# Kernel optimization log

Measured on AMD Instinct MI355X. Metric: run time of the kernel, lower is better.

The kernel has to match this reference:

```python
import jax, jax.numpy as jnp
import numpy as np

# Config from the repo: 128^3 volume, patch 2 -> 64^3 patches, embed_dim 64
D = H = W = 64
C = 64
WS = 2        # window_size
SS = 1        # shift_size
NH = 8        # num_heads
MLP = 256     # num_mlp
B = 2
L = D * H * W
S = WS ** 3   # tokens per window = 8
NUM_REL = (2 * WS - 1) ** 3  # 27


def _rel_position_index(ws):
    # faithful to source, incl. np.meshgrid default 'xy' indexing
    coords = np.stack(np.meshgrid(np.arange(ws), np.arange(ws), np.arange(ws)))
    cf = coords.reshape(3, -1)
    rc = (cf[:, :, None] - cf[:, None, :]).transpose(1, 2, 0)
    rc[:, :, 0] += ws - 1
    rc[:, :, 1] += ws - 1
    rc[:, :, 2] += ws - 1
    rc[:, :, 0] *= 2 * ws - 1
    return rc.sum(-1)  # (S, S) int


def _attn_mask(d, h, w, ws, ss):
    sl = (slice(0, -ws), slice(-ws, -ss), slice(-ss, None))
    m = np.zeros((1, d, h, w, 1), np.float32)
    cnt = 0
    for ds in sl:
        for hs in sl:
            for wsl in sl:
                m[:, ds, hs, wsl, :] = cnt
                cnt += 1
    pz, py, px = d // ws, h // ws, w // ws
    mw = m.reshape(1, pz, ws, py, ws, px, ws, 1)
    mw = mw.transpose(0, 1, 3, 5, 2, 4, 6, 7).reshape(-1, ws ** 3)  # (nW, S)
    am = mw[:, None, :] - mw[:, :, None]
    return np.where(am != 0, -100.0, 0.0).astype(np.float32)  # (nW, S, S)


_REL_IDX = _rel_position_index(WS).reshape(-1)          # (S*S,)
_MASK = _attn_mask(D, H, W, WS, SS)                     # (nW, S, S)


def setup_inputs() -> dict:
    key = jax.random.key(0)
    ks = jax.random.split(key, 8)
    n = lambda k, s: jax.random.normal(k, s, jnp.float32) * 0.02
    return {
        "x": jax.random.normal(ks[0], (B, L, C), jnp.float32),
        "norm1_g": jnp.ones((C,), jnp.float32),
        "norm1_b": jnp.zeros((C,), jnp.float32),
        "qkv_w": n(ks[1], (C, 3 * C)),
        "qkv_b": jnp.zeros((3 * C,), jnp.float32),
        "rpb": n(ks[2], (NUM_REL, NH)),
        "proj_w": n(ks[3], (C, C)),
        "proj_b": jnp.zeros((C,), jnp.float32),
        "norm2_g": jnp.ones((C,), jnp.float32),
        "norm2_b": jnp.zeros((C,), jnp.float32),
        "mlp_w1": n(ks[4], (C, MLP)),
        "mlp_b1": jnp.zeros((MLP,), jnp.float32),
        "mlp_w2": n(ks[5], (MLP, C)),
        "mlp_b2": jnp.zeros((C,), jnp.float32),
    }


def _ln(x, g, b, eps=1e-5):
    mu = jnp.mean(x, -1, keepdims=True)
    var = jnp.mean(jnp.square(x - mu), -1, keepdims=True)
    return (x - mu) * jax.lax.rsqrt(var + eps) * g + b


def _forward(x, norm1_g, norm1_b, qkv_w, qkv_b, rpb, proj_w, proj_b,
             norm2_g, norm2_b, mlp_w1, mlp_b1, mlp_w2, mlp_b2):
    b = x.shape[0]
    pz, py, px = D // WS, H // WS, W // WS
    hd = C // NH
    scale = hd ** -0.5

    h = _ln(x, norm1_g, norm1_b).reshape(b, D, H, W, C)
    h = jnp.roll(h, (-SS, -SS, -SS), (1, 2, 3))  # cyclic shift
    # window partition -> (b*nW, S, C)
    w = h.reshape(b, pz, WS, py, WS, px, WS, C)
    w = w.transpose(0, 1, 3, 5, 2, 4, 6, 7).reshape(-1, S, C)
    n = w.shape[0]

    qkv = (w @ qkv_w + qkv_b).reshape(n, S, 3, NH, hd).transpose(2, 0, 3, 1, 4)
    q, k, v = qkv[0] * scale, qkv[1], qkv[2]   # (n, NH, S, hd)
    attn = jnp.einsum('nhqd,nhkd->nhqk', q, k)  # (n, NH, S, S)

    # relative position bias, gather + reshape exactly as in the source
    bias = rpb[jnp.asarray(_REL_IDX)].reshape(S, S, S, -1).transpose(3, 0, 1, 2)
    attn = attn + bias  # broadcasts since NH == S == 8 in this config

    mask = jnp.asarray(_MASK)  # (nW, S, S)
    nW = mask.shape[0]
    attn = attn.reshape(-1, nW, NH, S, S) + mask[None, :, None]
    attn = jax.nn.softmax(attn.reshape(-1, NH, S, S), axis=-1)

    out = jnp.einsum('nhqk,nhkd->nhqd', attn, v)
    out = out.transpose(0, 2, 1, 3).reshape(n, S, C)
    out = out @ proj_w + proj_b

    # window reverse (bug-faithful to the source's reshape/transpose order)
    xr = out.reshape(-1, pz, WS, py, px, WS, WS, C)
    xr = xr.transpose(0, 1, 3, 5, 2, 4, 6, 7).reshape(-1, D, H, W, C)
    xr = jnp.roll(xr, (SS, SS, SS), (1, 2, 3))
    h = xr.reshape(b, L, C)

    x = x + h  # DropPath/Dropout are identity in eval mode
    skip = x
    h = _ln(x, norm2_g, norm2_b)
    h = jax.nn.gelu(h @ mlp_w1 + mlp_b1, approximate=False) @ mlp_w2 + mlp_b2
    return skip + h


def reference(x, norm1_g, norm1_b, qkv_w, qkv_b, rpb, proj_w, proj_b,
              norm2_g, norm2_b, mlp_w1, mlp_b1, mlp_w2, mlp_b2):
    return _forward(x, norm1_g, norm1_b, qkv_w, qkv_b, rpb, proj_w, proj_b,
                    norm2_g, norm2_b, mlp_w1, mlp_b1, mlp_w2, mlp_b2)
```

## Files before the change

### kernel.cpp

```cpp
#include <hip/hip_runtime.h>
#include <math.h>

typedef unsigned short u16;
typedef unsigned int u32;
typedef __attribute__((ext_vector_type(8))) short short8;
typedef __attribute__((ext_vector_type(4))) float f32x4;

__device__ __forceinline__ float bf2f(u16 u) {
  union { u32 i; float f; } v; v.i = ((u32)u) << 16; return v.f;
}
__device__ __forceinline__ u16 f2bf(float f) {
  union { float f; u32 i; } v; v.f = f;
  u32 i = v.i;
  i += 0x7fffu + ((i >> 16) & 1u);
  return (u16)(i >> 16);
}

template<bool F32>
__device__ __forceinline__ float ld(const void* p, int i) {
  if (F32) return ((const float*)p)[i];
  return bf2f(((const u16*)p)[i]);
}

__global__ __launch_bounds__(64)
void detect_kernel(const void* __restrict__ xv, int* __restrict__ flag) {
  const u32* xw = (const u32*)xv;
  const int t = threadIdx.x;
  int bad = 0;
  for (int i = t; i < 1024; i += 64) {
    const int e = (int)((xw[i] >> 7) & 0xFF);
    if (e < 90 || e > 150) bad++;
  }
#pragma unroll
  for (int m = 1; m < 64; m <<= 1) bad += __shfl_xor(bad, m);
  if (t == 0) *flag = (bad > 256) ? 1 : 0;
}

template<bool F32>
__device__ __forceinline__ void gather8(const void* __restrict__ x, int chunk,
                                        int w, int s, int cg, float* pf) {
  const int b     = chunk >> 13;
  const int wbase = (chunk & 8191) << 2;
  const int widx  = wbase + w;
  const int wz = widx >> 10, wy = (widx >> 5) & 31, wx = widx & 31;
  const int od = (2*wz + ((s>>2)&1) + 1) & 63;
  const int oh = (2*wy + ((s>>1)&1) + 1) & 63;
  const int ow = (2*wx + ( s    &1) + 1) & 63;
  const int base = (((b<<18) + ((od<<12)|(oh<<6)|ow)) << 6) + cg*8;
  if (F32) {
    const f32x4 a = *(const f32x4*)((const float*)x + base);
    const f32x4 c = *(const f32x4*)((const float*)x + base + 4);
    pf[0]=a[0]; pf[1]=a[1]; pf[2]=a[2]; pf[3]=a[3];
    pf[4]=c[0]; pf[5]=c[1]; pf[6]=c[2]; pf[7]=c[3];
  } else {
    const short8 a = *(const short8*)((const u16*)x + base);
#pragma unroll
    for (int j = 0; j < 8; ++j) pf[j] = bf2f((u16)a[j]);
  }
}

__device__ __forceinline__ int scat(int wbase, int b, int tok) {
  const int widx = wbase + (tok >> 3);
  const int s    = tok & 7;
  const int wz = widx >> 10, wy = (widx >> 5) & 31, wx = widx & 31;
  const int fd = (2*wz + ((wy>>3)&1) + 1) & 63;
  const int Hb = 8*(wy&7) + 4*(wx>>4) + (wy>>4);
  const int Wb = 4*(wx&15);
  const int i = (s>>2)&1, j = (s>>1)&1, k = s&1;
  const int fh = (Hb + 2*j + 1) & 63;
  const int fw = (Wb + 2*i + k + 1) & 63;
  return ((b<<18) + ((fd<<12)|(fh<<6)|fw)) << 6;
}

#define MFMA __builtin_amdgcn_mfma_f32_16x16x32_bf16

template<bool F32>
__device__ __forceinline__ void attn_body(
    const void* __restrict__ x,
    const void* __restrict__ n1g, const void* __restrict__ n1b,
    const void* __restrict__ qkvw, const void* __restrict__ qkvb,
    const void* __restrict__ rpb,
    const void* __restrict__ projw, const void* __restrict__ projb,
    float* __restrict__ out,
    u16* __restrict__ aL, u16* __restrict__ qL,
    u16* __restrict__ kL, u16* __restrict__ vL)
{
  const int tid  = threadIdx.x;
  const int w    = tid >> 6, l = tid & 63;
  const int quad = l >> 4,  col = l & 15;
  const int s8   = l >> 3,  cg  = l & 7;

  float g1v[8], be1v[8];
#pragma unroll
  for (int j = 0; j < 8; ++j) {
    g1v[j]  = ld<F32>(n1g, cg*8 + j);
    be1v[j] = ld<F32>(n1b, cg*8 + j);
  }

  short8 bq[3][2];
#pragma unroll
  for (int nt = 0; nt < 3; ++nt)
#pragma unroll
    for (int kt = 0; kt < 2; ++kt) {
      short8 f;
#pragma unroll
      for (int j = 0; j < 8; ++j)
        f[j] = (short)f2bf(ld<F32>(qkvw, (kt*32 + quad*8 + j)*192 + w*48 + nt*16 + col));
      bq[nt][kt] = f;
    }
  float qb[3];
#pragma unroll
  for (int nt = 0; nt < 3; ++nt) qb[nt] = ld<F32>(qkvb, w*48 + nt*16 + col);
  short8 bp[2];
#pragma unroll
  for (int kt = 0; kt < 2; ++kt) {
    short8 f;
#pragma unroll
    for (int j = 0; j < 8; ++j)
      f[j] = (short)f2bf(ld<F32>(projw, (kt*32 + quad*8 + j)*64 + w*16 + col));
    bp[kt] = f;
  }
  const float pbv = ld<F32>(projb, w*16 + col);
  const int rel = 3 * (((s8>>1)&1) - ((cg>>1)&1) + 1)
                +     (((s8>>2)&1) - ((cg>>2)&1) + 1)
                +     (( s8    &1) - ( cg    &1) + 1);

  float pf[8];
  gather8<F32>(x, blockIdx.x, w, s8, cg, pf);

  for (int chunk = blockIdx.x; chunk < 16384; chunk += 2048) {
    const int b     = chunk >> 13;
    const int wbase = (chunk & 8191) << 2;
    const int widx0 = wbase + w;
    const int wz0 = widx0 >> 10, wy0 = (widx0 >> 5) & 31, wx0 = widx0 & 31;

    {
      float s1 = 0.f, sq = 0.f;
#pragma unroll
      for (int j = 0; j < 8; ++j) { s1 += pf[j]; sq += pf[j]*pf[j]; }
#pragma unroll
      for (int m = 1; m < 8; m <<= 1) {
        s1 += __shfl_xor(s1, m);
        sq += __shfl_xor(sq, m);
      }
      const float mu  = s1 * 0.015625f;
      const float var = sq * 0.015625f - mu * mu;
      const float rs  = rsqrtf(var + 1e-5f);
      short8 av;
#pragma unroll
      for (int j = 0; j < 8; ++j)
        av[j] = (short)f2bf((pf[j] - mu) * rs * g1v[j] + be1v[j]);
      *(short8*)&aL[(w*8 + s8)*72 + cg*8] = av;
    }
    if (chunk + 2048 < 16384) gather8<F32>(x, chunk + 2048, w, s8, cg, pf);
    __syncthreads();

    {
      short8 aF[2][2];
#pragma unroll
      for (int mt = 0; mt < 2; ++mt)
#pragma unroll
        for (int kt = 0; kt < 2; ++kt)
          aF[mt][kt] = *(const short8*)&aL[(mt*16 + col)*72 + kt*32 + quad*8];
#pragma unroll
      for (int nt = 0; nt < 3; ++nt) {
        f32x4 a0 = (f32x4){0.f,0.f,0.f,0.f}, a1 = (f32x4){0.f,0.f,0.f,0.f};
        a0 = MFMA(aF[0][0], bq[nt][0], a0, 0, 0, 0);
        a0 = MFMA(aF[0][1], bq[nt][1], a0, 0, 0, 0);
        a1 = MFMA(aF[1][0], bq[nt][0], a1, 0, 0, 0);
        a1 = MFMA(aF[1][1], bq[nt][1], a1, 0, 0, 0);
        const int nb  = w*48 + nt*16;
        u16* dst      = (nb < 64) ? qL : (nb < 128) ? kL : vL;
        const int chb = (nb & 63) + col;
        const float scl = (nb < 64) ? 0.35355339059327373f : 1.0f;
        const float bb  = qb[nt];
#pragma unroll
        for (int r = 0; r < 4; ++r) {
          dst[(quad*4 + r)*72 + chb]      = f2bf((a0[r] + bb) * scl);
          dst[(16 + quad*4 + r)*72 + chb] = f2bf((a1[r] + bb) * scl);
        }
      }
    }
    __syncthreads();

    {
      const int tq = w*8 + cg;
      float qr[8];
      {
        const short8 qv = *(const short8*)&qL[tq*72 + s8*8];
#pragma unroll
        for (int d = 0; d < 8; ++d) qr[d] = bf2f((u16)qv[d]);
      }
      float sc8[8];
#pragma unroll
      for (int kk = 0; kk < 8; ++kk) {
        const short8 kv = *(const short8*)&kL[(w*8 + kk)*72 + s8*8];
        float a = 0.f;
#pragma unroll
        for (int d = 0; d < 8; ++d) a += qr[d] * bf2f((u16)kv[d]);
        sc8[kk] = a + ld<F32>(rpb, rel*8 + kk);
      }
      {
        int cnts[8];
#pragma unroll
        for (int p = 0; p < 8; ++p) {
          const int sd = 2*wz0 + ((p>>2)&1);
          const int sh = 2*wy0 + ((p>>1)&1);
          const int sw = 2*wx0 + (p&1);
          cnts[p] = (sd >= 62 ? sd - 61 : 0)*9 + (sh >= 62 ? sh - 61 : 0)*3
                  + (sw >= 62 ? sw - 61 : 0);
        }
#pragma unroll
        for (int kk = 0; kk < 8; ++kk)
          if (cnts[kk] != cnts[cg]) sc8[kk] -= 100.f;
      }
      float mx = sc8[0];
#pragma unroll
      for (int kk = 1; kk < 8; ++kk) mx = fmaxf(mx, sc8[kk]);
      float pr[8], lsum = 0.f;
#pragma unroll
      for (int kk = 0; kk < 8; ++kk) { pr[kk] = __expf(sc8[kk] - mx); lsum += pr[kk]; }
      const float inv = __builtin_amdgcn_rcpf(lsum);
      float o[8];
#pragma unroll
      for (int d = 0; d < 8; ++d) o[d] = 0.f;
#pragma unroll
      for (int kk = 0; kk < 8; ++kk) {
        const short8 vv = *(const short8*)&vL[(w*8 + kk)*72 + s8*8];
#pragma unroll
        for (int d = 0; d < 8; ++d) o[d] += pr[kk] * bf2f((u16)vv[d]);
      }
      short8 ov;
#pragma unroll
      for (int d = 0; d < 8; ++d) ov[d] = (short)f2bf(o[d] * inv);
      *(short8*)&qL[tq*72 + s8*8] = ov;
    }
    int offs[8]; float xr[8];
#pragma unroll
    for (int mt = 0; mt < 2; ++mt)
#pragma unroll
      for (int r = 0; r < 4; ++r) {
        const int off = scat(wbase, b, mt*16 + quad*4 + r) + w*16 + col;
        offs[mt*4 + r] = off;
        xr[mt*4 + r]   = ld<F32>(x, off);
      }
    __syncthreads();

    {
      f32x4 c0 = (f32x4){0.f,0.f,0.f,0.f}, c1 = (f32x4){0.f,0.f,0.f,0.f};
      c0 = MFMA(*(const short8*)&qL[(col)*72 + quad*8],         bp[0], c0, 0, 0, 0);
      c0 = MFMA(*(const short8*)&qL[(col)*72 + 32 + quad*8],    bp[1], c0, 0, 0, 0);
      c1 = MFMA(*(const short8*)&qL[(16+col)*72 + quad*8],      bp[0], c1, 0, 0, 0);
      c1 = MFMA(*(const short8*)&qL[(16+col)*72 + 32 + quad*8], bp[1], c1, 0, 0, 0);
#pragma unroll
      for (int r = 0; r < 4; ++r) {
        out[offs[r]]     = xr[r]     + c0[r] + pbv;
        out[offs[4 + r]] = xr[4 + r] + c1[r] + pbv;
      }
    }
    __syncthreads();
  }
}

__global__ __launch_bounds__(256, 4)
void attn_kernel(const void* __restrict__ x,
                 const void* __restrict__ n1g, const void* __restrict__ n1b,
                 const void* __restrict__ qkvw, const void* __restrict__ qkvb,
                 const void* __restrict__ rpb,
                 const void* __restrict__ projw, const void* __restrict__ projb,
                 const int* __restrict__ flag, float* __restrict__ out)
{
  __shared__ __align__(16) u16 aL[32*72];
  __shared__ __align__(16) u16 qL[32*72];
  __shared__ __align__(16) u16 kL[32*72];
  __shared__ __align__(16) u16 vL[32*72];
  if (*flag)
    attn_body<true >(x, n1g, n1b, qkvw, qkvb, rpb, projw, projb, out, aL, qL, kL, vL);
  else
    attn_body<false>(x, n1g, n1b, qkvw, qkvb, rpb, projw, projb, out, aL, qL, kL, vL);
}

template<bool F32>
__device__ __forceinline__ void mlp_body(
    float* __restrict__ io,
    const void* __restrict__ n2g, const void* __restrict__ n2b,
    const void* __restrict__ mw1, const void* __restrict__ mb1,
    const void* __restrict__ mw2, const void* __restrict__ mb2,
    u16* __restrict__ aL, u16* __restrict__ hL, float* __restrict__ yL)
{
  const int tid  = threadIdx.x;
  const int w    = tid >> 6, l = tid & 63;
  const int quad = l >> 4,  col = l & 15;
  const int s8   = l >> 3,  cg  = l & 7;
  const int ltok = w*8 + s8;

  float g2v[8], be2v[8];
#pragma unroll
  for (int j = 0; j < 8; ++j) {
    g2v[j]  = ld<F32>(n2g, cg*8 + j);
    be2v[j] = ld<F32>(n2b, cg*8 + j);
  }

  short8 b1f[2][4];
#pragma unroll
  for (int kt = 0; kt < 2; ++kt)
#pragma unroll
    for (int nt = 0; nt < 4; ++nt) {
      short8 f;
#pragma unroll
      for (int j = 0; j < 8; ++j)
        f[j] = (short)f2bf(ld<F32>(mw1, (kt*32 + quad*8 + j)*256 + w*64 + nt*16 + col));
      b1f[kt][nt] = f;
    }
  short8 b2f[8];
#pragma unroll
  for (int kt = 0; kt < 8; ++kt) {
    short8 f;
#pragma unroll
    for (int j = 0; j < 8; ++j)
      f[j] = (short)f2bf(ld<F32>(mw2, (kt*32 + quad*8 + j)*64 + w*16 + col));
    b2f[kt] = f;
  }
  float b1vv[4];
#pragma unroll
  for (int nt = 0; nt < 4; ++nt) b1vv[nt] = ld<F32>(mb1, w*64 + nt*16 + col);
  const float b2vv = ld<F32>(mb2, w*16 + col);

  float pf[8];
  {
    const float* p = &io[(blockIdx.x*32 + ltok)*64 + cg*8];
    const f32x4 a = *(const f32x4*)p;
    const f32x4 c = *(const f32x4*)(p + 4);
    pf[0]=a[0]; pf[1]=a[1]; pf[2]=a[2]; pf[3]=a[3];
    pf[4]=c[0]; pf[5]=c[1]; pf[6]=c[2]; pf[7]=c[3];
  }

  for (int chunk = blockIdx.x; chunk < 16384; chunk += 2048) {
    {
      float s1 = 0.f, sq = 0.f;
#pragma unroll
      for (int j = 0; j < 8; ++j) { s1 += pf[j]; sq += pf[j]*pf[j]; }
#pragma unroll
      for (int m = 1; m < 8; m <<= 1) {
        s1 += __shfl_xor(s1, m);
        sq += __shfl_xor(sq, m);
      }
      const float mu  = s1 * 0.015625f;
      const float var = sq * 0.015625f - mu * mu;
      const float rs  = rsqrtf(var + 1e-5f);
      short8 av;
#pragma unroll
      for (int j = 0; j < 8; ++j)
        av[j] = (short)f2bf((pf[j] - mu) * rs * g2v[j] + be2v[j]);
      *(short8*)&aL[ltok*72 + cg*8] = av;
      *(f32x4*)&yL[ltok*68 + cg*8]     = (f32x4){pf[0], pf[1], pf[2], pf[3]};
      *(f32x4*)&yL[ltok*68 + cg*8 + 4] = (f32x4){pf[4], pf[5], pf[6], pf[7]};
    }
    if (chunk + 2048 < 16384) {
      const float* p = &io[((chunk + 2048)*32 + ltok)*64 + cg*8];
      const f32x4 a = *(const f32x4*)p;
      const f32x4 c = *(const f32x4*)(p + 4);
      pf[0]=a[0]; pf[1]=a[1]; pf[2]=a[2]; pf[3]=a[3];
      pf[4]=c[0]; pf[5]=c[1]; pf[6]=c[2]; pf[7]=c[3];
    }
    __syncthreads();

    {
      short8 aF[2][2];
#pragma unroll
      for (int mt = 0; mt < 2; ++mt)
#pragma unroll
        for (int kt = 0; kt < 2; ++kt)
          aF[mt][kt] = *(const short8*)&aL[(mt*16 + col)*72 + kt*32 + quad*8];
#pragma unroll
      for (int nt = 0; nt < 4; ++nt) {
        f32x4 m0 = (f32x4){0.f,0.f,0.f,0.f}, m1 = (f32x4){0.f,0.f,0.f,0.f};
        m0 = MFMA(aF[0][0], b1f[0][nt], m0, 0, 0, 0);
        m0 = MFMA(aF[0][1], b1f[1][nt], m0, 0, 0, 0);
        m1 = MFMA(aF[1][0], b1f[0][nt], m1, 0, 0, 0);
        m1 = MFMA(aF[1][1], b1f[1][nt], m1, 0, 0, 0);
        const float bb = b1vv[nt];
#pragma unroll
        for (int r = 0; r < 4; ++r) {
          {
            const float h = m0[r] + bb;
            const float u = h * (1.5957691216f + 0.0713548162f * (h * h));
            const float e = __expf(u);
            hL[(quad*4 + r)*264 + w*64 + nt*16 + col] =
                f2bf(h - h * __builtin_amdgcn_rcpf(e + 1.f));
          }
          {
            const float h = m1[r] + bb;
            const float u = h * (1.5957691216f + 0.0713548162f * (h * h));
            const float e = __expf(u);
            hL[(16 + quad*4 + r)*264 + w*64 + nt*16 + col] =
                f2bf(h - h * __builtin_amdgcn_rcpf(e + 1.f));
          }
        }
      }
    }
    __syncthreads();

    {
      f32x4 o0 = (f32x4){0.f,0.f,0.f,0.f}, o1 = (f32x4){0.f,0.f,0.f,0.f};
#pragma unroll
      for (int kt = 0; kt < 8; ++kt) {
        o0 = MFMA(*(const short8*)&hL[(col)*264 + kt*32 + quad*8],    b2f[kt], o0, 0, 0, 0);
        o1 = MFMA(*(const short8*)&hL[(16+col)*264 + kt*32 + quad*8], b2f[kt], o1, 0, 0, 0);
      }
#pragma unroll
      for (int r = 0; r < 4; ++r) {
        const int r0 = quad*4 + r, r1 = 16 + quad*4 + r;
        io[(chunk*32 + r0)*64 + w*16 + col] = yL[r0*68 + w*16 + col] + o0[r] + b2vv;
        io[(chunk*32 + r1)*64 + w*16 + col] = yL[r1*68 + w*16 + col] + o1[r] + b2vv;
      }
    }
    __syncthreads();
  }
}

__global__ __launch_bounds__(256, 4)
void mlp_kernel(float* __restrict__ io,
                const void* __restrict__ n2g, const void* __restrict__ n2b,
                const void* __restrict__ mw1, const void* __restrict__ mb1,
                const void* __restrict__ mw2, const void* __restrict__ mb2,
                const int* __restrict__ flag)
{
  __shared__ __align__(16) u16   aL[32 * 72];
  __shared__ __align__(16) u16   hL[32 * 264];
  __shared__ __align__(16) float yL[32 * 68];
  if (*flag)
    mlp_body<true >(io, n2g, n2b, mw1, mb1, mw2, mb2, aL, hL, yL);
  else
    mlp_body<false>(io, n2g, n2b, mw1, mb1, mw2, mb2, aL, hL, yL);
}

extern "C" void kernel_launch(void* const* d_in, const int* in_sizes, int n_in,
                              void* d_out, int out_size, void* d_ws, size_t ws_size,
                              hipStream_t stream) {
  const void* x     = d_in[0];
  const void* n1g   = d_in[1];
  const void* n1b   = d_in[2];
  const void* qkvw  = d_in[3];
  const void* qkvb  = d_in[4];
  const void* rpb   = d_in[5];
  const void* projw = d_in[6];
  const void* projb = d_in[7];
  const void* n2g   = d_in[8];
  const void* n2b   = d_in[9];
  const void* mw1   = d_in[10];
  const void* mb1   = d_in[11];
  const void* mw2   = d_in[12];
  const void* mb2   = d_in[13];
  float* out = (float*)d_out;
  int* flag  = (int*)d_ws;

  detect_kernel<<<dim3(1), dim3(64), 0, stream>>>(x, flag);
  attn_kernel<<<dim3(2048), dim3(256), 0, stream>>>(
      x, n1g, n1b, qkvw, qkvb, rpb, projw, projb, flag, out);
  mlp_kernel<<<dim3(2048), dim3(256), 0, stream>>>(
      out, n2g, n2b, mw1, mb1, mw2, mb2, flag);
}
```

Before: 445.8 us.

## Fuse attention and MLP kernels into one persistent kernel

Merges the attention and MLP kernels into a single kernel, so the post-attention residual stays in shared memory and the MLP runs on it directly. This removes the intermediate global write and read of the full activation tensor plus one launch. Output is written with vectorized stores per token at the scattered location, and the residual x is gathered per token with vector loads. LayerNorm params and rel-pos bias move into shared memory. In exchange it holds more weight registers and more shared memory (launch bounds lowered to 3 blocks/CU), which may reduce occupancy.

```diff
diff --git a/kernel.cpp b/kernel.cpp
--- a/kernel.cpp
+++ b/kernel.cpp
@@ -59,7 +59,9 @@
   }
 }
 
-__device__ __forceinline__ int scat(int wbase, int b, int tok) {
+__device__ __forceinline__ int scat(int chunk, int tok) {
+  const int b     = chunk >> 13;
+  const int wbase = (chunk & 8191) << 2;
   const int widx = wbase + (tok >> 3);
   const int s    = tok & 7;
   const int wz = widx >> 10, wy = (widx >> 5) & 31, wx = widx & 31;
@@ -72,29 +74,57 @@
   return ((b<<18) + ((fd<<12)|(fh<<6)|fw)) << 6;
 }
 
+template<bool F32>
+__device__ __forceinline__ void loadx8(const void* __restrict__ x, int base,
+                                       float* xr) {
+  if (F32) {
+    const f32x4 a = *(const f32x4*)((const float*)x + base);
+    const f32x4 c = *(const f32x4*)((const float*)x + base + 4);
+    xr[0]=a[0]; xr[1]=a[1]; xr[2]=a[2]; xr[3]=a[3];
+    xr[4]=c[0]; xr[5]=c[1]; xr[6]=c[2]; xr[7]=c[3];
+  } else {
+    const short8 a = *(const short8*)((const u16*)x + base);
+#pragma unroll
+    for (int j = 0; j < 8; ++j) xr[j] = bf2f((u16)a[j]);
+  }
+}
+
 #define MFMA __builtin_amdgcn_mfma_f32_16x16x32_bf16
 
 template<bool F32>
-__device__ __forceinline__ void attn_body(
+__device__ __forceinline__ void fused_body(
     const void* __restrict__ x,
     const void* __restrict__ n1g, const void* __restrict__ n1b,
     const void* __restrict__ qkvw, const void* __restrict__ qkvb,
     const void* __restrict__ rpb,
     const void* __restrict__ projw, const void* __restrict__ projb,
-    float* __restrict__ out,
-    u16* __restrict__ aL, u16* __restrict__ qL,
-    u16* __restrict__ kL, u16* __restrict__ vL)
+    const void* __restrict__ n2g, const void* __restrict__ n2b,
+    const void* __restrict__ mw1, const void* __restrict__ mb1,
+    const void* __restrict__ mw2, const void* __restrict__ mb2,
+    float* __restrict__ out, u16* __restrict__ P)
 {
+  u16* aL   = P;
+  u16* qL   = P + 2304;
+  u16* kL   = P + 4608;
+  u16* vL   = P + 6912;
+  u16* hL   = P + 2304;
+  float* yL = (float*)(P + 10752);
+  float* xL = (float*)(P + 15104);
+  float* oL = xL;
+  float* pL = (float*)(P + 19456);
+  float* rpL = pL + 256;
+
   const int tid  = threadIdx.x;
   const int w    = tid >> 6, l = tid & 63;
   const int quad = l >> 4,  col = l & 15;
   const int s8   = l >> 3,  cg  = l & 7;
-
-  float g1v[8], be1v[8];
-#pragma unroll
-  for (int j = 0; j < 8; ++j) {
-    g1v[j]  = ld<F32>(n1g, cg*8 + j);
-    be1v[j] = ld<F32>(n1b, cg*8 + j);
+  const int tok_l = w*8 + s8;
+
+  {
+    const int a = tid >> 6, c = tid & 63;
+    const void* src = (a==0) ? n1g : (a==1) ? n1b : (a==2) ? n2g : n2b;
+    pL[tid] = ld<F32>(src, c);
+    if (tid < 216) rpL[tid] = ld<F32>(rpb, tid);
   }
 
   short8 bq[3][2];
@@ -121,15 +151,44 @@
     bp[kt] = f;
   }
   const float pbv = ld<F32>(projb, w*16 + col);
+  short8 b1f[2][4];
+#pragma unroll
+  for (int kt = 0; kt < 2; ++kt)
+#pragma unroll
+    for (int nt = 0; nt < 4; ++nt) {
+      short8 f;
+#pragma unroll
+      for (int j = 0; j < 8; ++j)
+        f[j] = (short)f2bf(ld<F32>(mw1, (kt*32 + quad*8 + j)*256 + w*64 + nt*16 + col));
+      b1f[kt][nt] = f;
+    }
+  short8 b2f[8];
+#pragma unroll
+  for (int kt = 0; kt < 8; ++kt) {
+    short8 f;
+#pragma unroll
+    for (int j = 0; j < 8; ++j)
+      f[j] = (short)f2bf(ld<F32>(mw2, (kt*32 + quad*8 + j)*64 + w*16 + col));
+    b2f[kt] = f;
+  }
+  float b1v[4];
+#pragma unroll
+  for (int nt = 0; nt < 4; ++nt) b1v[nt] = ld<F32>(mb1, w*64 + nt*16 + col);
+  const float b2v = ld<F32>(mb2, w*16 + col);
+
   const int rel = 3 * (((s8>>1)&1) - ((cg>>1)&1) + 1)
                 +     (((s8>>2)&1) - ((cg>>2)&1) + 1)
                 +     (( s8    &1) - ( cg    &1) + 1);
 
-  float pf[8];
+  __syncthreads();
+
+  const int G = gridDim.x;
+  float pf[8], xr[8];
+  int off_c = scat(blockIdx.x, tok_l) + cg*8;
   gather8<F32>(x, blockIdx.x, w, s8, cg, pf);
-
-  for (int chunk = blockIdx.x; chunk < 16384; chunk += 2048) {
-    const int b     = chunk >> 13;
+  loadx8<F32>(x, off_c, xr);
+
+  for (int chunk = blockIdx.x; chunk < 16384; chunk += G) {
     const int wbase = (chunk & 8191) << 2;
     const int widx0 = wbase + w;
     const int wz0 = widx0 >> 10, wy0 = (widx0 >> 5) & 31, wx0 = widx0 & 31;
@@ -149,10 +208,17 @@
       short8 av;
 #pragma unroll
       for (int j = 0; j < 8; ++j)
-        av[j] = (short)f2bf((pf[j] - mu) * rs * g1v[j] + be1v[j]);
-      *(short8*)&aL[(w*8 + s8)*72 + cg*8] = av;
-    }
-    if (chunk + 2048 < 16384) gather8<F32>(x, chunk + 2048, w, s8, cg, pf);
+        av[j] = (short)f2bf((pf[j] - mu) * rs * pL[cg*8 + j] + pL[64 + cg*8 + j]);
+      *(short8*)&aL[tok_l*72 + cg*8] = av;
+      *(f32x4*)&xL[tok_l*68 + cg*8]     = (f32x4){xr[0], xr[1], xr[2], xr[3]};
+      *(f32x4*)&xL[tok_l*68 + cg*8 + 4] = (f32x4){xr[4], xr[5], xr[6], xr[7]};
+    }
+    int off_n = off_c;
+    if (chunk + G < 16384) {
+      gather8<F32>(x, chunk + G, w, s8, cg, pf);
+      off_n = scat(chunk + G, tok_l) + cg*8;
+      loadx8<F32>(x, off_n, xr);
+    }
     __syncthreads();
 
     {
@@ -198,7 +264,7 @@
         float a = 0.f;
 #pragma unroll
         for (int d = 0; d < 8; ++d) a += qr[d] * bf2f((u16)kv[d]);
-        sc8[kk] = a + ld<F32>(rpb, rel*8 + kk);
+        sc8[kk] = a + rpL[rel*8 + kk];
       }
       {
         int cnts[8];
@@ -235,15 +301,6 @@
       for (int d = 0; d < 8; ++d) ov[d] = (short)f2bf(o[d] * inv);
       *(short8*)&qL[tq*72 + s8*8] = ov;
     }
-    int offs[8]; float xr[8];
-#pragma unroll
-    for (int mt = 0; mt < 2; ++mt)
-#pragma unroll
-      for (int r = 0; r < 4; ++r) {
-        const int off = scat(wbase, b, mt*16 + quad*4 + r) + w*16 + col;
-        offs[mt*4 + r] = off;
-        xr[mt*4 + r]   = ld<F32>(x, off);
-      }
     __syncthreads();
 
     {
@@ -254,92 +311,22 @@
       c1 = MFMA(*(const short8*)&qL[(16+col)*72 + 32 + quad*8], bp[1], c1, 0, 0, 0);
 #pragma unroll
       for (int r = 0; r < 4; ++r) {
-        out[offs[r]]     = xr[r]     + c0[r] + pbv;
-        out[offs[4 + r]] = xr[4 + r] + c1[r] + pbv;
-      }
-    }
-    __syncthreads();
-  }
-}
-
-__global__ __launch_bounds__(256, 4)
-void attn_kernel(const void* __restrict__ x,
-                 const void* __restrict__ n1g, const void* __restrict__ n1b,
-                 const void* __restrict__ qkvw, const void* __restrict__ qkvb,
-                 const void* __restrict__ rpb,
-                 const void* __restrict__ projw, const void* __restrict__ projb,
-                 const int* __restrict__ flag, float* __restrict__ out)
-{
-  __shared__ __align__(16) u16 aL[32*72];
-  __shared__ __align__(16) u16 qL[32*72];
-  __shared__ __align__(16) u16 kL[32*72];
-  __shared__ __align__(16) u16 vL[32*72];
-  if (*flag)
-    attn_body<true >(x, n1g, n1b, qkvw, qkvb, rpb, projw, projb, out, aL, qL, kL, vL);
-  else
-    attn_body<false>(x, n1g, n1b, qkvw, qkvb, rpb, projw, projb, out, aL, qL, kL, vL);
-}
-
-template<bool F32>
-__device__ __forceinline__ void mlp_body(
-    float* __restrict__ io,
-    const void* __restrict__ n2g, const void* __restrict__ n2b,
-    const void* __restrict__ mw1, const void* __restrict__ mb1,
-    const void* __restrict__ mw2, const void* __restrict__ mb2,
-    u16* __restrict__ aL, u16* __restrict__ hL, float* __restrict__ yL)
-{
-  const int tid  = threadIdx.x;
-  const int w    = tid >> 6, l = tid & 63;
-  const int quad = l >> 4,  col = l & 15;
-  const int s8   = l >> 3,  cg  = l & 7;
-  const int ltok = w*8 + s8;
-
-  float g2v[8], be2v[8];
-#pragma unroll
-  for (int j = 0; j < 8; ++j) {
-    g2v[j]  = ld<F32>(n2g, cg*8 + j);
-    be2v[j] = ld<F32>(n2b, cg*8 + j);
-  }
-
-  short8 b1f[2][4];
-#pragma unroll
-  for (int kt = 0; kt < 2; ++kt)
-#pragma unroll
-    for (int nt = 0; nt < 4; ++nt) {
-      short8 f;
-#pragma unroll
-      for (int j = 0; j < 8; ++j)
-        f[j] = (short)f2bf(ld<F32>(mw1, (kt*32 + quad*8 + j)*256 + w*64 + nt*16 + col));
-      b1f[kt][nt] = f;
-    }
-  short8 b2f[8];
-#pragma unroll
-  for (int kt = 0; kt < 8; ++kt) {
-    short8 f;
-#pragma unroll
-    for (int j = 0; j < 8; ++j)
-      f[j] = (short)f2bf(ld<F32>(mw2, (kt*32 + quad*8 + j)*64 + w*16 + col));
-    b2f[kt] = f;
-  }
-  float b1vv[4];
-#pragma unroll
-  for (int nt = 0; nt < 4; ++nt) b1vv[nt] = ld<F32>(mb1, w*64 + nt*16 + col);
-  const float b2vv = ld<F32>(mb2, w*16 + col);
-
-  float pf[8];
-  {
-    const float* p = &io[(blockIdx.x*32 + ltok)*64 + cg*8];
-    const f32x4 a = *(const f32x4*)p;
-    const f32x4 c = *(const f32x4*)(p + 4);
-    pf[0]=a[0]; pf[1]=a[1]; pf[2]=a[2]; pf[3]=a[3];
-    pf[4]=c[0]; pf[5]=c[1]; pf[6]=c[2]; pf[7]=c[3];
-  }
-
-  for (int chunk = blockIdx.x; chunk < 16384; chunk += 2048) {
-    {
+        const int r0 = quad*4 + r, r1 = 16 + quad*4 + r;
+        yL[r0*68 + w*16 + col] = xL[r0*68 + w*16 + col] + c0[r] + pbv;
+        yL[r1*68 + w*16 + col] = xL[r1*68 + w*16 + col] + c1[r] + pbv;
+      }
+    }
+    __syncthreads();
+
+    {
+      float yv[8];
+      const f32x4 a = *(const f32x4*)&yL[tok_l*68 + cg*8];
+      const f32x4 c = *(const f32x4*)&yL[tok_l*68 + cg*8 + 4];
+      yv[0]=a[0]; yv[1]=a[1]; yv[2]=a[2]; yv[3]=a[3];
+      yv[4]=c[0]; yv[5]=c[1]; yv[6]=c[2]; yv[7]=c[3];
       float s1 = 0.f, sq = 0.f;
 #pragma unroll
-      for (int j = 0; j < 8; ++j) { s1 += pf[j]; sq += pf[j]*pf[j]; }
+      for (int j = 0; j < 8; ++j) { s1 += yv[j]; sq += yv[j]*yv[j]; }
 #pragma unroll
       for (int m = 1; m < 8; m <<= 1) {
         s1 += __shfl_xor(s1, m);
@@ -351,17 +338,8 @@
       short8 av;
 #pragma unroll
       for (int j = 0; j < 8; ++j)
-        av[j] = (short)f2bf((pf[j] - mu) * rs * g2v[j] + be2v[j]);
-      *(short8*)&aL[ltok*72 + cg*8] = av;
-      *(f32x4*)&yL[ltok*68 + cg*8]     = (f32x4){pf[0], pf[1], pf[2], pf[3]};
-      *(f32x4*)&yL[ltok*68 + cg*8 + 4] = (f32x4){pf[4], pf[5], pf[6], pf[7]};
-    }
-    if (chunk + 2048 < 16384) {
-      const float* p = &io[((chunk + 2048)*32 + ltok)*64 + cg*8];
-      const f32x4 a = *(const f32x4*)p;
-      const f32x4 c = *(const f32x4*)(p + 4);
-      pf[0]=a[0]; pf[1]=a[1]; pf[2]=a[2]; pf[3]=a[3];
-      pf[4]=c[0]; pf[5]=c[1]; pf[6]=c[2]; pf[7]=c[3];
+        av[j] = (short)f2bf((yv[j] - mu) * rs * pL[128 + cg*8 + j] + pL[192 + cg*8 + j]);
+      *(short8*)&aL[tok_l*72 + cg*8] = av;
     }
     __syncthreads();
 
@@ -379,7 +357,7 @@
         m0 = MFMA(aF[0][1], b1f[1][nt], m0, 0, 0, 0);
         m1 = MFMA(aF[1][0], b1f[0][nt], m1, 0, 0, 0);
         m1 = MFMA(aF[1][1], b1f[1][nt], m1, 0, 0, 0);
-        const float bb = b1vv[nt];
+        const float bb = b1v[nt];
 #pragma unroll
         for (int r = 0; r < 4; ++r) {
           {
@@ -411,28 +389,46 @@
 #pragma unroll
       for (int r = 0; r < 4; ++r) {
         const int r0 = quad*4 + r, r1 = 16 + quad*4 + r;
-        io[(chunk*32 + r0)*64 + w*16 + col] = yL[r0*68 + w*16 + col] + o0[r] + b2vv;
-        io[(chunk*32 + r1)*64 + w*16 + col] = yL[r1*68 + w*16 + col] + o1[r] + b2vv;
-      }
-    }
-    __syncthreads();
-  }
-}
-
-__global__ __launch_bounds__(256, 4)
-void mlp_kernel(float* __restrict__ io,
-                const void* __restrict__ n2g, const void* __restrict__ n2b,
-                const void* __restrict__ mw1, const void* __restrict__ mb1,
-                const void* __restrict__ mw2, const void* __restrict__ mb2,
-                const int* __restrict__ flag)
+        oL[r0*68 + w*16 + col] = o0[r] + b2v;
+        oL[r1*68 + w*16 + col] = o1[r] + b2v;
+      }
+    }
+    __syncthreads();
+
+    {
+      const f32x4 ya = *(const f32x4*)&yL[tok_l*68 + cg*8];
+      const f32x4 yb = *(const f32x4*)&yL[tok_l*68 + cg*8 + 4];
+      const f32x4 oa = *(const f32x4*)&oL[tok_l*68 + cg*8];
+      const f32x4 ob = *(const f32x4*)&oL[tok_l*68 + cg*8 + 4];
+      f32x4 sa, sb;
+#pragma unroll
+      for (int j = 0; j < 4; ++j) { sa[j] = ya[j] + oa[j]; sb[j] = yb[j] + ob[j]; }
+      *(f32x4*)&out[off_c]     = sa;
+      *(f32x4*)&out[off_c + 4] = sb;
+    }
+    __syncthreads();
+    off_c = off_n;
+  }
+}
+
+__global__ __launch_bounds__(256, 3)
+void fused_kernel(const void* __restrict__ x,
+                  const void* __restrict__ n1g, const void* __restrict__ n1b,
+                  const void* __restrict__ qkvw, const void* __restrict__ qkvb,
+                  const void* __restrict__ rpb,
+                  const void* __restrict__ projw, const void* __restrict__ projb,
+                  const void* __restrict__ n2g, const void* __restrict__ n2b,
+                  const void* __restrict__ mw1, const void* __restrict__ mb1,
+                  const void* __restrict__ mw2, const void* __restrict__ mb2,
+                  const int* __restrict__ flag, float* __restrict__ out)
 {
-  __shared__ __align__(16) u16   aL[32 * 72];
-  __shared__ __align__(16) u16   hL[32 * 264];
-  __shared__ __align__(16) float yL[32 * 68];
+  __shared__ __align__(16) u16 P[20400];
   if (*flag)
-    mlp_body<true >(io, n2g, n2b, mw1, mb1, mw2, mb2, aL, hL, yL);
+    fused_body<true >(x, n1g, n1b, qkvw, qkvb, rpb, projw, projb,
+                      n2g, n2b, mw1, mb1, mw2, mb2, out, P);
   else
-    mlp_body<false>(io, n2g, n2b, mw1, mb1, mw2, mb2, aL, hL, yL);
+    fused_body<false>(x, n1g, n1b, qkvw, qkvb, rpb, projw, projb,
+                      n2g, n2b, mw1, mb1, mw2, mb2, out, P);
 }
 
 extern "C" void kernel_launch(void* const* d_in, const int* in_sizes, int n_in,
@@ -456,8 +452,7 @@
   int* flag  = (int*)d_ws;
 
   detect_kernel<<<dim3(1), dim3(64), 0, stream>>>(x, flag);
-  attn_kernel<<<dim3(2048), dim3(256), 0, stream>>>(
-      x, n1g, n1b, qkvw, qkvb, rpb, projw, projb, flag, out);
-  mlp_kernel<<<dim3(2048), dim3(256), 0, stream>>>(
-      out, n2g, n2b, mw1, mb1, mw2, mb2, flag);
-}
+  fused_kernel<<<dim3(2048), dim3(256), 0, stream>>>(
+      x, n1g, n1b, qkvw, qkvb, rpb, projw, projb,
+      n2g, n2b, mw1, mb1, mw2, mb2, flag, out);
+}
```

After: 680.4 us. 52.6% more time.
